# Performance work log

Hardware: AMD Instinct MI355X
Metric: run time of the kernel (lower is better)

Reference implementation:

```python
import jax, jax.numpy as jnp
import numpy as np

# Module hyperparameters derived from init_kwargs
G = 100          # grid_size = int(n_samples ** gamma) = int(10000 ** 0.5)
K = 3            # KAN_SPLINE_ORDER
NB = G + K       # num_basis = 103
H = (1.5 - (-0.5)) / G
# grid identical for every input feature (torch expands a 1D grid)
GRID = jnp.arange(-K, G + K + 1, dtype=jnp.float32) * H - 0.5  # (G + 2K + 1,)


def bspline_basis(x):
    """Cox-de Boor recursion. x: (B, F) -> (B, F, NB)."""
    g = GRID
    xe = x[..., None]  # (B, F, 1)
    bases = ((xe >= g[:-1]) & (xe < g[1:])).astype(x.dtype)  # (B, F, G+2K)
    for k in range(1, K + 1):
        left = (xe - g[:-(k + 1)]) / jnp.maximum(g[k:-1] - g[:-(k + 1)], 1e-8)
        right = (g[k + 1:] - xe) / jnp.maximum(g[k + 1:] - g[1:-k], 1e-8)
        bases = left * bases[..., :-1] + right * bases[..., 1:]
    return bases  # (B, F, NB)


def kan_layer(x, bw, sw, wb, ws, residual):
    # base path: SiLU activation then linear
    base_out = jax.nn.silu(x) @ bw.T                      # (B, out)
    # spline path: basis expansion then contraction with spline_weight
    spline_out = jnp.einsum('bin,oin->bo', bspline_basis(x), sw)
    out = wb * base_out + ws * spline_out
    return out + x if residual else out


def setup_inputs() -> dict:
    key = jax.random.key(0)
    ks = jax.random.split(key, 16)
    B, D, W = 2048, 64, 243
    inp = {'x': jax.random.uniform(ks[0], (B, D), dtype=jnp.float32)}
    dims = [(D, W), (W, W), (W, W), (W, W), (W, W), (W, 1)]
    for i, (fi, fo) in enumerate(dims):
        kb, ksw = jax.random.split(jax.random.fold_in(key, i + 1))
        inp[f'bw{i}'] = jax.random.normal(kb, (fo, fi), dtype=jnp.float32) * (1.0 / np.sqrt(fi))
        # torch init: uniform(-0.5/G, 0.5/G)
        inp[f'sw{i}'] = jax.random.uniform(ksw, (fo, fi, NB), dtype=jnp.float32,
                                           minval=-0.5 / G, maxval=0.5 / G)
        inp[f'wb{i}'] = jnp.zeros((1,), dtype=jnp.float32)
        inp[f'ws{i}'] = jnp.ones((1,), dtype=jnp.float32)
    return inp


def reference(x, bw0, sw0, wb0, ws0, bw1, sw1, wb1, ws1, bw2, sw2, wb2, ws2,
              bw3, sw3, wb3, ws3, bw4, sw4, wb4, ws4, bw5, sw5, wb5, ws5):
    layers = [
        (bw0, sw0, wb0, ws0, False),  # 64 -> 243 (in != out: no residual)
        (bw1, sw1, wb1, ws1, True),
        (bw2, sw2, wb2, ws2, True),
        (bw3, sw3, wb3, ws3, True),
        (bw4, sw4, wb4, ws4, True),
        (bw5, sw5, wb5, ws5, False),  # 243 -> 1 (use_residual=False)
    ]
    h = x
    for bw, sw, wb, ws, res in layers:
        h = kan_layer(h, bw, sw, wb, ws, res)
    return h
```

## Files before the change

kernel.cpp:

```cpp
#include <hip/hip_runtime.h>
#include <hip/hip_fp16.h>
#include <math.h>

#define BATCH 2048
#define NBAS 103
#define NPAIR 102
#define OUTR 243
#define OUTP 256

typedef _Float16 half2v __attribute__((ext_vector_type(2)));

__device__ __forceinline__ float dot2(unsigned a, unsigned b, float c) {
#if __has_builtin(__builtin_amdgcn_fdot2)
    return __builtin_amdgcn_fdot2(__builtin_bit_cast(half2v, a),
                                  __builtin_bit_cast(half2v, b), c, false);
#else
    __half2 ha = __builtin_bit_cast(__half2, a), hb = __builtin_bit_cast(__half2, b);
    c = fmaf(__low2float(ha), __low2float(hb), c);
    c = fmaf(__high2float(ha), __high2float(hb), c);
    return c;
#endif
}

__device__ __forceinline__ uint4 make_meta(float x, int i) {
    float u = (x + 0.56f) * 50.0f;
    bool inr = (u >= 0.0f) && (u < 106.0f);
    float fj = floorf(u);
    float t = u - fj;
    int j = (int)fj;
    j = j < -1 ? -1 : (j > 106 ? 106 : j);
    float omt = 1.0f - t;
    float t2 = t * t, t3 = t2 * t;
    float w[4];
    w[0] = omt * omt * omt * (1.0f / 6.0f);
    w[1] = (3.0f * t3 - 6.0f * t2 + 4.0f) * (1.0f / 6.0f);
    w[2] = (-3.0f * t3 + 3.0f * t2 + 3.0f * t + 1.0f) * (1.0f / 6.0f);
    w[3] = t3 * (1.0f / 6.0f);
    int idx = j - 3;
    int idxc = idx < 0 ? 0 : (idx > 99 ? 99 : idx);
    int d = idx - idxc;
    float wc[4];
    #pragma unroll
    for (int m = 0; m < 4; ++m) {
        int s = m - d;
        wc[m] = (inr && s >= 0 && s < 4) ? w[s] : 0.0f;
    }
    __half2 w01 = __floats2half2_rn(wc[0], wc[1]);
    __half2 w23 = __floats2half2_rn(wc[2], wc[3]);
    uint4 m4;
    m4.x = __builtin_bit_cast(unsigned, w01);
    m4.y = __builtin_bit_cast(unsigned, w23);
    m4.z = (unsigned)((i * (NPAIR * 4) + idxc) << 6);
    m4.w = (unsigned)(i * NBAS + idxc);
    return m4;
}

__device__ __forceinline__ void pairgen_body64(
    const float* __restrict__ sw, int IN, unsigned* __restrict__ pairT,
    __half (*tile)[106], int i, int obase)
{
    int nl = threadIdx.x & 63;
    int w = threadIdx.x >> 6;
    #pragma unroll
    for (int k = 0; k < 16; ++k) {
        int r = w * 16 + k;
        int o = obase + r;
        if (o < OUTR) {
            const float* p = sw + ((size_t)o * IN + i) * NBAS;
            tile[r][nl] = __float2half(p[nl]);
            if (nl + 64 < NBAS)
                tile[r][nl + 64] = __float2half(p[nl + 64]);
        } else {
            tile[r][nl] = __ushort_as_half((unsigned short)0);
            if (nl + 64 < 106)
                tile[r][nl + 64] = __ushort_as_half((unsigned short)0);
        }
    }
    __syncthreads();
    int ol = threadIdx.x & 63;
    int rg = threadIdx.x >> 6;
    unsigned* dst = pairT + (size_t)i * (NPAIR * 4 * 64) + (size_t)(obase >> 6) * (NPAIR * 64);
    for (int r = 0; r < NPAIR; r += 4) {
        int rr = r + rg;
        if (rr < NPAIR) {
            unsigned lo = __half_as_ushort(tile[ol][rr]);
            unsigned hi = __half_as_ushort(tile[ol][rr + 1]);
            dst[(size_t)rr * 64 + ol] = lo | (hi << 16);
        }
    }
}

__global__ __launch_bounds__(256) void pairgen_kernel(
    const float* __restrict__ sw, int IN, unsigned* __restrict__ pairT)
{
    __shared__ __half tile[64][106];
    pairgen_body64(sw, IN, pairT, tile, blockIdx.x, blockIdx.y * 64);
}

__global__ __launch_bounds__(256) void front_kernel(
    const float* __restrict__ sw0, unsigned* __restrict__ pT0,
    const float* __restrict__ sw1, unsigned* __restrict__ pT1,
    const float* __restrict__ xin, uint4* __restrict__ meta)
{
    int bx = blockIdx.x;
    if (bx < 1228) {
        __shared__ __half tile[64][106];
        if (bx < 256) pairgen_body64(sw0, 64, pT0, tile, bx >> 2, (bx & 3) * 64);
        else {
            int t = bx - 256;
            pairgen_body64(sw1, OUTR, pT1, tile, t >> 2, (t & 3) * 64);
        }
    } else {
        int e = (bx - 1228) * 256 + threadIdx.x;
        int b = e >> 6, i = e & 63;
        meta[e] = make_meta(xin[(size_t)b * 64 + i], i);
    }
}

template <int IN>
__global__ __launch_bounds__(256) void basis_kernel(
    const float* __restrict__ xin, int xstride, uint4* __restrict__ meta,
    float4* __restrict__ zbuf)
{
    int e = blockIdx.x * 256 + threadIdx.x;
    if (zbuf && e < (BATCH * OUTP) / 4) zbuf[e] = make_float4(0.f, 0.f, 0.f, 0.f);
    if (e >= BATCH * IN) return;
    int b = e / IN, i = e - b * IN;
    meta[e] = make_meta(xin[(size_t)b * xstride + i], i);
}

template <bool ADDRES>
__global__ __launch_bounds__(256) void basis_mid_kernel(
    const float* __restrict__ hprev,
    const float* __restrict__ parts,
    uint4* __restrict__ meta, float* __restrict__ hcomb)
{
    int e = blockIdx.x * 256 + threadIdx.x;
    if (e >= BATCH * OUTR) return;
    int b = e / OUTR, i = e - b * OUTR;
    size_t addr = (size_t)b * OUTP + i;
    const size_t PS = (size_t)BATCH * OUTP;
    float h = ADDRES ? hprev[addr] : 0.0f;
    #pragma unroll
    for (int s = 0; s < 8; ++s) h += parts[s * PS + addr];
    hcomb[addr] = h;
    meta[e] = make_meta(h, i);
}

template <bool ADDRES>
__global__ __launch_bounds__(256) void fused_pg_bm_kernel(
    const float* __restrict__ sw, unsigned* __restrict__ pairT,
    const float* __restrict__ hprev, const float* __restrict__ parts,
    uint4* __restrict__ meta, float* __restrict__ hcomb)
{
    if (blockIdx.y == 0) {
        __shared__ __half tile[64][106];
        if (blockIdx.x < 972)
            pairgen_body64(sw, OUTR, pairT, tile, blockIdx.x >> 2, (blockIdx.x & 3) * 64);
    } else {
        int e = blockIdx.x * 256 + threadIdx.x;
        if (e >= BATCH * OUTR) return;
        int b = e / OUTR, i = e - b * OUTR;
        size_t addr = (size_t)b * OUTP + i;
        const size_t PS = (size_t)BATCH * OUTP;
        float h = ADDRES ? hprev[addr] : 0.0f;
        #pragma unroll
        for (int s = 0; s < 8; ++s) h += parts[s * PS + addr];
        hcomb[addr] = h;
        meta[e] = make_meta(h, i);
    }
}

__global__ __launch_bounds__(256) void fused0_kernel(
    const float* __restrict__ sw0, unsigned* __restrict__ pairT,
    const float* __restrict__ xin, uint4* __restrict__ meta)
{
    if (blockIdx.y == 0) {
        __shared__ __half tile[64][106];
        if (blockIdx.x < 256)
            pairgen_body64(sw0, 64, pairT, tile, blockIdx.x >> 2, (blockIdx.x & 3) * 64);
    } else {
        int e = blockIdx.x * 256 + threadIdx.x;
        int b = e >> 6, i = e & 63;
        meta[e] = make_meta(xin[(size_t)b * 64 + i], i);
    }
}

template <int IN>
__device__ __forceinline__ void ls_body(
    const unsigned* __restrict__ pairT, const uint4* __restrict__ meta,
    const float* __restrict__ h_in, int hstride,
    const float* __restrict__ bw,
    const float* __restrict__ wbp, const float* __restrict__ wsp,
    float* __restrict__ part, int cx, int by)
{
    const int lane = threadIdx.x & 63;
    const int wave = __builtin_amdgcn_readfirstlane(threadIdx.x >> 6);
    const int b0 = by * 16 + wave * 4;
    const int i0 = (IN * cx) >> 3;
    const int i1 = (IN * (cx + 1)) >> 3;
    const unsigned laneoff = ((unsigned)(lane >> 4) * (NPAIR * 64)) + ((unsigned)(lane & 15) << 2);
    const uint4* mp = meta + (size_t)b0 * IN;
    float a[4][4] = {};
    #pragma unroll 2
    for (int i = i0; i < i1; ++i) {
        uint4 m[4];
        #pragma unroll
        for (int r = 0; r < 4; ++r) m[r] = mp[(size_t)r * IN + i];
        uint4 lo[4], hi[4];
        #pragma unroll
        for (int r = 0; r < 4; ++r) {
            const uint4* p = (const uint4*)(pairT + m[r].z + laneoff);
            lo[r] = p[0];
            hi[r] = p[32];
        }
        #pragma unroll
        for (int r = 0; r < 4; ++r) {
            a[r][0] = dot2(m[r].x, lo[r].x, a[r][0]);
            a[r][1] = dot2(m[r].x, lo[r].y, a[r][1]);
            a[r][2] = dot2(m[r].x, lo[r].z, a[r][2]);
            a[r][3] = dot2(m[r].x, lo[r].w, a[r][3]);
            a[r][0] = dot2(m[r].y, hi[r].x, a[r][0]);
            a[r][1] = dot2(m[r].y, hi[r].y, a[r][1]);
            a[r][2] = dot2(m[r].y, hi[r].z, a[r][2]);
            a[r][3] = dot2(m[r].y, hi[r].w, a[r][3]);
        }
    }
    float wsv = wsp[0];
    float wbv = wbp[0];
    #pragma unroll
    for (int r = 0; r < 4; ++r) {
        float4 v = make_float4(wsv * a[r][0], wsv * a[r][1], wsv * a[r][2], wsv * a[r][3]);
        if (wbv != 0.0f) {
            float* pv = &v.x;
            for (int c = 0; c < 4; ++c) {
                int o = lane * 4 + c;
                if (o < OUTR) {
                    float bs = 0.0f;
                    for (int i = i0; i < i1; ++i) {
                        float xx = h_in[(size_t)(b0 + r) * hstride + i];
                        bs = fmaf(xx / (1.0f + expf(-xx)), bw[o * IN + i], bs);
                    }
                    pv[c] += wbv * bs;
                }
            }
        }
        float* d = part + ((size_t)cx * BATCH + b0 + r) * OUTP + lane * 4;
        *(float4*)d = v;
    }
}

template <int IN>
__global__ __launch_bounds__(256, 4) void layer_store_kernel(
    const unsigned* __restrict__ pairT, const uint4* __restrict__ meta,
    const float* __restrict__ h_in, int hstride,
    const float* __restrict__ bw,
    const float* __restrict__ wbp, const float* __restrict__ wsp,
    float* __restrict__ part)
{
    ls_body<IN>(pairT, meta, h_in, hstride, bw, wbp, wsp, part, blockIdx.x, blockIdx.y);
}

__global__ __launch_bounds__(256, 4) void ls_pg_kernel(
    const unsigned* __restrict__ pairT, const uint4* __restrict__ meta,
    const float* __restrict__ h_in, int hstride,
    const float* __restrict__ bw,
    const float* __restrict__ wbp, const float* __restrict__ wsp,
    float* __restrict__ part,
    const float* __restrict__ sw_next, unsigned* __restrict__ pT_next)
{
    if (blockIdx.x < 8) {
        ls_body<OUTR>(pairT, meta, h_in, hstride, bw, wbp, wsp, part,
                      blockIdx.x, blockIdx.y);
    } else {
        __shared__ __half tile[64][106];
        int idx = (blockIdx.x - 8) + blockIdx.y * 8;
        if (idx < 972)
            pairgen_body64(sw_next, OUTR, pT_next, tile, idx >> 2, (idx & 3) * 64);
    }
}

template <int IN, bool RES>
__global__ __launch_bounds__(256, 8) void layer_atomic_kernel(
    const unsigned* __restrict__ pairT, const uint4* __restrict__ meta,
    const float* __restrict__ h_in, int hstride,
    const float* __restrict__ bw,
    const float* __restrict__ wbp, const float* __restrict__ wsp,
    float* __restrict__ out)
{
    const int lane = threadIdx.x & 63;
    const int wave = __builtin_amdgcn_readfirstlane(threadIdx.x >> 6);
    const int b = blockIdx.y * 4 + wave;
    const int cx = blockIdx.x;
    const int i0 = (IN * cx) >> 3;
    const int i1 = (IN * (cx + 1)) >> 3;
    const unsigned laneoff = ((unsigned)(lane >> 4) * (NPAIR * 64)) + ((unsigned)(lane & 15) << 2);
    const uint4* mp = meta + (size_t)b * IN;
    float acc[4] = {0.f, 0.f, 0.f, 0.f};
    #pragma unroll 2
    for (int i = i0; i < i1; ++i) {
        uint4 m = mp[i];
        const uint4* pA = (const uint4*)(pairT + m.z + laneoff);
        uint4 ra = pA[0];
        uint4 rb = pA[32];
        acc[0] = dot2(m.x, ra.x, acc[0]); acc[1] = dot2(m.x, ra.y, acc[1]);
        acc[2] = dot2(m.x, ra.z, acc[2]); acc[3] = dot2(m.x, ra.w, acc[3]);
        acc[0] = dot2(m.y, rb.x, acc[0]); acc[1] = dot2(m.y, rb.y, acc[1]);
        acc[2] = dot2(m.y, rb.z, acc[2]); acc[3] = dot2(m.y, rb.w, acc[3]);
    }
    float wsv = wsp[0];
    float wbv = wbp[0];
    #pragma unroll
    for (int c = 0; c < 4; ++c) {
        int o = lane * 4 + c;
        float v = wsv * acc[c];
        if (RES && cx == 0) v += h_in[(size_t)b * hstride + o];
        if (wbv != 0.0f && o < OUTR) {
            float bs = 0.0f;
            for (int i = i0; i < i1; ++i) {
                float xx = h_in[(size_t)b * hstride + i];
                bs = fmaf(xx / (1.0f + expf(-xx)), bw[o * IN + i], bs);
            }
            v += wbv * bs;
        }
        unsafeAtomicAdd(&out[(size_t)b * OUTP + o], v);
    }
}

__global__ __launch_bounds__(256) void final_fused_kernel(
    const float* __restrict__ sw5,
    const float* __restrict__ hprev,
    const float* __restrict__ parts,
    const float* __restrict__ bw5,
    const float* __restrict__ wbp, const float* __restrict__ wsp,
    float* __restrict__ out)
{
    int wave = threadIdx.x >> 6, lane = threadIdx.x & 63;
    int b = blockIdx.x * 4 + wave;
    const size_t PS = (size_t)BATCH * OUTP;
    float s = 0.0f, bs = 0.0f;
    for (int i = lane; i < OUTR; i += 64) {
        size_t addr = (size_t)b * OUTP + i;
        float h = hprev[addr];
        #pragma unroll
        for (int ss = 0; ss < 8; ++ss) h += parts[ss * PS + addr];
        uint4 m = make_meta(h, i);
        __half2 w01 = __builtin_bit_cast(__half2, m.x);
        __half2 w23 = __builtin_bit_cast(__half2, m.y);
        const float* p = sw5 + m.w;
        s += __low2float(w01) * p[0] + __high2float(w01) * p[1]
           + __low2float(w23) * p[2] + __high2float(w23) * p[3];
        bs = fmaf(h / (1.0f + expf(-h)), bw5[i], bs);
    }
    #pragma unroll
    for (int d = 32; d; d >>= 1) {
        s += __shfl_down(s, d, 64);
        bs += __shfl_down(bs, d, 64);
    }
    if (lane == 0) out[b] = wsp[0] * s + wbp[0] * bs;
}

__global__ __launch_bounds__(256) void final_kernel(
    const float* __restrict__ sw5,
    const uint4* __restrict__ meta,
    const float* __restrict__ h, const float* __restrict__ bw5,
    const float* __restrict__ wbp, const float* __restrict__ wsp,
    float* __restrict__ out)
{
    int wave = threadIdx.x >> 6, lane = threadIdx.x & 63;
    int b = blockIdx.x * 4 + wave;
    float s = 0.0f;
    for (int i = lane; i < OUTR; i += 64) {
        uint4 m = meta[(size_t)b * OUTR + i];
        __half2 w01 = __builtin_bit_cast(__half2, m.x);
        __half2 w23 = __builtin_bit_cast(__half2, m.y);
        const float* p = sw5 + m.w;
        s += __low2float(w01) * p[0] + __high2float(w01) * p[1]
           + __low2float(w23) * p[2] + __high2float(w23) * p[3];
    }
    #pragma unroll
    for (int d = 32; d; d >>= 1) s += __shfl_down(s, d, 64);
    if (lane == 0) {
        float v = wsp[0] * s;
        float wbv = wbp[0];
        if (wbv != 0.0f) {
            float bs = 0.0f;
            for (int i = 0; i < OUTR; ++i) {
                float xx = h[(size_t)b * OUTP + i];
                bs = fmaf(xx / (1.0f + expf(-xx)), bw5[i], bs);
            }
            v += wbv * bs;
        }
        out[b] = v;
    }
}

extern "C" void kernel_launch(void* const* d_in, const int* in_sizes, int n_in,
                              void* d_out, int out_size, void* d_ws, size_t ws_size,
                              hipStream_t stream)
{
    const float* x = (const float*)d_in[0];
    const float *bw[6], *sw[6], *wb[6], *ws[6];
    for (int l = 0; l < 6; ++l) {
        bw[l] = (const float*)d_in[1 + 4 * l];
        sw[l] = (const float*)d_in[2 + 4 * l];
        wb[l] = (const float*)d_in[3 + 4 * l];
        ws[l] = (const float*)d_in[4 + 4 * l];
    }
    char* base = (char*)d_ws;
    float* outp = (float*)d_out;
    const int NB243 = (BATCH * OUTR + 255) / 256;

    const size_t NEED_ALL = 137142272;
    const size_t NEED_MID = 54315008;
    const size_t NEED_ATM = 37537792;

    if (ws_size >= NEED_ALL) {
        unsigned* T0 = (unsigned*)(base + 0);
        unsigned* T1 = (unsigned*)(base + 6684672);
        unsigned* T2 = (unsigned*)(base + 32065536);
        unsigned* T3 = (unsigned*)(base + 57446400);
        unsigned* T4 = (unsigned*)(base + 82827264);
        uint4*    meta  = (uint4*)(base + 108208128);
        float*    parts = (float*)(base + 116170752);
        float*    hcA   = (float*)(base + 132947968);
        float*    hcB   = (float*)(base + 135045120);
        unsigned* pT[5] = {T0, T1, T2, T3, T4};

        front_kernel<<<1740, 256, 0, stream>>>(sw[0], T0, sw[1], T1, x, meta);

        layer_store_kernel<64><<<dim3(8, BATCH / 16), 256, 0, stream>>>(
            T0, meta, x, 64, bw[0], wb[0], ws[0], parts);

        float* hin = hcA; float* hout = hcB;
        for (int l = 1; l <= 4; ++l) {
            if (l == 1)
                basis_mid_kernel<false><<<NB243, 256, 0, stream>>>(nullptr, parts, meta, hin);
            else
                basis_mid_kernel<true><<<NB243, 256, 0, stream>>>(hout, parts, meta, hin);
            if (l <= 3)
                ls_pg_kernel<<<dim3(16, BATCH / 16), 256, 0, stream>>>(
                    pT[l], meta, hin, OUTP, bw[l], wb[l], ws[l], parts,
                    sw[l + 1], pT[l + 1]);
            else
                layer_store_kernel<243><<<dim3(8, BATCH / 16), 256, 0, stream>>>(
                    pT[4], meta, hin, OUTP, bw[4], wb[4], ws[4], parts);
            float* tmp = hin; hin = hout; hout = tmp;
        }
        final_fused_kernel<<<BATCH / 4, 256, 0, stream>>>(
            sw[5], hout, parts, bw[5], wb[5], ws[5], outp);
    } else if (ws_size >= NEED_MID) {
        unsigned* pairT1 = (unsigned*)(base + 0);
        uint4*    meta   = (uint4*)(base + 25380864);
        float*    parts  = (float*)(base + 33343488);
        float*    hcA    = (float*)(base + 50120704);
        float*    hcB    = (float*)(base + 52217856);

        fused0_kernel<<<dim3(512, 2), 256, 0, stream>>>(sw[0], pairT1, x, meta);
        layer_store_kernel<64><<<dim3(8, BATCH / 16), 256, 0, stream>>>(
            pairT1, meta, x, 64, bw[0], wb[0], ws[0], parts);

        float* hin = hcA; float* hout = hcB;
        for (int l = 1; l <= 4; ++l) {
            if (l == 1)
                fused_pg_bm_kernel<false><<<dim3(1944, 2), 256, 0, stream>>>(
                    sw[l], pairT1, nullptr, parts, meta, hin);
            else
                fused_pg_bm_kernel<true><<<dim3(1944, 2), 256, 0, stream>>>(
                    sw[l], pairT1, hout, parts, meta, hin);
            layer_store_kernel<243><<<dim3(8, BATCH / 16), 256, 0, stream>>>(
                pairT1, meta, hin, OUTP, bw[l], wb[l], ws[l], parts);
            float* tmp = hin; hin = hout; hout = tmp;
        }
        final_fused_kernel<<<BATCH / 4, 256, 0, stream>>>(
            sw[5], hout, parts, bw[5], wb[5], ws[5], outp);
    } else {
        if (ws_size < NEED_ATM) return;
        unsigned* pairT1 = (unsigned*)(base + 0);
        uint4*    meta   = (uint4*)(base + 25380864);
        float* hA = (float*)(base + 33343488);
        float* hB = (float*)(base + 35440640);
        pairgen_kernel<<<dim3(64, 4), 256, 0, stream>>>(sw[0], 64, pairT1);
        basis_kernel<64><<<(BATCH * 64) / 256, 256, 0, stream>>>(x, 64, meta, (float4*)hA);
        layer_atomic_kernel<64, false><<<dim3(8, BATCH / 4), 256, 0, stream>>>(
            pairT1, meta, x, 64, bw[0], wb[0], ws[0], hA);
        float* hin = hA; float* hout = hB;
        for (int l = 1; l <= 4; ++l) {
            pairgen_kernel<<<dim3(OUTR, 4), 256, 0, stream>>>(sw[l], OUTR, pairT1);
            basis_kernel<243><<<NB243, 256, 0, stream>>>(hin, OUTP, meta, (float4*)hout);
            layer_atomic_kernel<243, true><<<dim3(8, BATCH / 4), 256, 0, stream>>>(
                pairT1, meta, hin, OUTP, bw[l], wb[l], ws[l], hout);
            float* tmp = hin; hin = hout; hout = tmp;
        }
        basis_kernel<243><<<NB243, 256, 0, stream>>>(hin, OUTP, meta, nullptr);
        final_kernel<<<BATCH / 4, 256, 0, stream>>>(sw[5], meta, hin, bw[5], wb[5], ws[5], outp);
    }
}
```

Measured before the change: 442.0 us.

## Move next-layer pair generation into basis-mid kernel and remap pairgen block indices

```diff
diff --git a/kernel.cpp b/kernel.cpp
--- a/kernel.cpp
+++ b/kernel.cpp
@@ -105,10 +105,12 @@
     int bx = blockIdx.x;
     if (bx < 1228) {
         __shared__ __half tile[64][106];
-        if (bx < 256) pairgen_body64(sw0, 64, pT0, tile, bx >> 2, (bx & 3) * 64);
-        else {
+        if (bx < 256) {
+            pairgen_body64(sw0, 64, pT0, tile, bx & 63, (bx >> 6) * 64);
+        } else {
             int t = bx - 256;
-            pairgen_body64(sw1, OUTR, pT1, tile, t >> 2, (t & 3) * 64);
+            int ot = t / 243, i = t - ot * 243;
+            pairgen_body64(sw1, OUTR, pT1, tile, i, ot * 64);
         }
     } else {
         int e = (bx - 1228) * 256 + threadIdx.x;
@@ -155,8 +157,10 @@
 {
     if (blockIdx.y == 0) {
         __shared__ __half tile[64][106];
-        if (blockIdx.x < 972)
-            pairgen_body64(sw, OUTR, pairT, tile, blockIdx.x >> 2, (blockIdx.x & 3) * 64);
+        if (blockIdx.x < 972) {
+            int ot = blockIdx.x / 243, i = blockIdx.x - ot * 243;
+            pairgen_body64(sw, OUTR, pairT, tile, i, ot * 64);
+        }
     } else {
         int e = blockIdx.x * 256 + threadIdx.x;
         if (e >= BATCH * OUTR) return;
@@ -178,7 +182,7 @@
     if (blockIdx.y == 0) {
         __shared__ __half tile[64][106];
         if (blockIdx.x < 256)
-            pairgen_body64(sw0, 64, pairT, tile, blockIdx.x >> 2, (blockIdx.x & 3) * 64);
+            pairgen_body64(sw0, 64, pairT, tile, blockIdx.x & 63, (blockIdx.x >> 6) * 64);
     } else {
         int e = blockIdx.x * 256 + threadIdx.x;
         int b = e >> 6, i = e & 63;
@@ -261,25 +265,6 @@
     ls_body<IN>(pairT, meta, h_in, hstride, bw, wbp, wsp, part, blockIdx.x, blockIdx.y);
 }
 
-__global__ __launch_bounds__(256, 4) void ls_pg_kernel(
-    const unsigned* __restrict__ pairT, const uint4* __restrict__ meta,
-    const float* __restrict__ h_in, int hstride,
-    const float* __restrict__ bw,
-    const float* __restrict__ wbp, const float* __restrict__ wsp,
-    float* __restrict__ part,
-    const float* __restrict__ sw_next, unsigned* __restrict__ pT_next)
-{
-    if (blockIdx.x < 8) {
-        ls_body<OUTR>(pairT, meta, h_in, hstride, bw, wbp, wsp, part,
-                      blockIdx.x, blockIdx.y);
-    } else {
-        __shared__ __half tile[64][106];
-        int idx = (blockIdx.x - 8) + blockIdx.y * 8;
-        if (idx < 972)
-            pairgen_body64(sw_next, OUTR, pT_next, tile, idx >> 2, (idx & 3) * 64);
-    }
-}
-
 template <int IN, bool RES>
 __global__ __launch_bounds__(256, 8) void layer_atomic_kernel(
     const unsigned* __restrict__ pairT, const uint4* __restrict__ meta,
@@ -437,14 +422,10 @@
             if (l == 1)
                 basis_mid_kernel<false><<<NB243, 256, 0, stream>>>(nullptr, parts, meta, hin);
             else
-                basis_mid_kernel<true><<<NB243, 256, 0, stream>>>(hout, parts, meta, hin);
-            if (l <= 3)
-                ls_pg_kernel<<<dim3(16, BATCH / 16), 256, 0, stream>>>(
-                    pT[l], meta, hin, OUTP, bw[l], wb[l], ws[l], parts,
-                    sw[l + 1], pT[l + 1]);
-            else
-                layer_store_kernel<243><<<dim3(8, BATCH / 16), 256, 0, stream>>>(
-                    pT[4], meta, hin, OUTP, bw[4], wb[4], ws[4], parts);
+                fused_pg_bm_kernel<true><<<dim3(1944, 2), 256, 0, stream>>>(
+                    sw[l], pT[l], hout, parts, meta, hin);
+            layer_store_kernel<243><<<dim3(8, BATCH / 16), 256, 0, stream>>>(
+                pT[l], meta, hin, OUTP, bw[l], wb[l], ws[l], parts);
             float* tmp = hin; hin = hout; hout = tmp;
         }
         final_fused_kernel<<<BATCH / 4, 256, 0, stream>>>(
```

New measurement: 429.1 us. -2.9%, faster.
